# Kernel tuning notes

Hardware: AMD Instinct MI355X
Metric: run time of the kernel (lower is better)

The kernel has to match this reference:

```python
import jax, jax.numpy as jnp
import numpy as np

G, BATCH, L, S_D, I_D, O_D = 2, 128, 2048, 64, 16, 16
SNR = 10.0


def _stable_F(key):
    # mirror utils.sample_stable_state_matrix: random matrix with spectral radius < 1
    A = jax.random.normal(key, (G, S_D, S_D), jnp.float32)
    sig_max = jnp.linalg.svd(A, compute_uv=False)[..., 0]  # spectral norm >= spectral radius
    return 0.95 * A / sig_max[:, None, None]


def setup_inputs() -> dict:
    key = jax.random.key(0)
    ks = jax.random.split(key, 9)
    return {
        "state": jax.random.normal(ks[0], (G, BATCH, S_D), jnp.float32),
        "inputs": jax.random.normal(ks[1], (G, BATCH, L, I_D), jnp.float32),
        "F": _stable_F(ks[2]),
        "B_mat": jax.random.normal(ks[3], (G, S_D, I_D), jnp.float32),
        "H": jax.random.normal(ks[4], (G, O_D, S_D), jnp.float32),
        "sqrt_S_W": jax.random.normal(ks[5], (G, S_D, S_D), jnp.float32) / SNR,
        "sqrt_S_V": jax.random.normal(ks[6], (G, O_D, O_D), jnp.float32) / SNR,
        "w_noise": jax.random.normal(ks[7], (L, G, BATCH, S_D), jnp.float32),
        "v_noise": jax.random.normal(ks[8], (L, G, BATCH, O_D), jnp.float32),
    }


def reference(state, inputs, F, B_mat, H, sqrt_S_W, sqrt_S_V, w_noise, v_noise):
    # Color the noise: randn @ sqrt_S.mT, as in the torch forward
    W = jnp.einsum('lgbs,gts->lgbt', w_noise, sqrt_S_W)   # [L,G,B,S_D]
    V = jnp.einsum('lgbo,gpo->lgbp', v_noise, sqrt_S_V)   # [L,G,B,O_D]
    # Precompute input drive for every step: inputs_ @ B.mT
    Bu = jnp.einsum('gbli,gsi->lgbs', inputs, B_mat)      # [L,G,B,S_D]

    def step(s, xs):
        Bu_t, W_t, V_t = xs
        s = jnp.einsum('gbs,gts->gbt', s, F) + Bu_t + W_t  # state @ F.mT + u @ B.mT + W
        o = jnp.einsum('gbs,gos->gbo', s, H) + V_t         # state @ H.mT + V
        return s, (s, o)

    _, (states, observations) = jax.lax.scan(step, state, (Bu, W, V))
    # [L,G,B,D] -> [G,B,L,D] to match torch.stack(..., dim=-2)
    states = jnp.moveaxis(states, 0, -2)
    observations = jnp.moveaxis(observations, 0, -2)
    return states, observations
```

## Files before the change

### kernel.cpp

```cpp
#include <hip/hip_runtime.h>

#define G_ 2
#define B_ 128
#define L_ 2048
#define SD 64
#define ID 16
#define OD 16
#define NC4 512
#define OBS_BASE ((size_t)(G_) * B_ * L_ * SD)

typedef float v2 __attribute__((ext_vector_type(2)));

static __device__ __forceinline__ size_t slotof(int g, int b, int l) {
  return (((size_t)g * B_ + b) * L_ + l) * (size_t)SD;
}
static __device__ __forceinline__ size_t oslot(int g, int b, int c4) {
  return OBS_BASE + (((size_t)g * B_ + b) * L_ + (size_t)c4 * 4) * OD;
}
static __device__ __forceinline__ float rl(float v, int lane) {
  return __builtin_bit_cast(float, __builtin_amdgcn_readlane(__builtin_bit_cast(int, v), lane));
}
static __device__ __forceinline__ void lds_barrier() {
  asm volatile("s_waitcnt lgkmcnt(0)\n\ts_barrier" ::: "memory");
}

static __device__ void lds_sq(const float* A, float* C, int tid) {
  const int r = tid & 63, q = tid >> 6;
  const float4* Ar = (const float4*)(A + r * SD);
  float acc[16];
#pragma unroll
  for (int c = 0; c < 16; ++c) acc[c] = 0.f;
#pragma unroll 1
  for (int k4 = 0; k4 < 16; ++k4) {
    float4 af = Ar[k4];
    const float* Bb = A + k4 * 4 * SD + q * 16;
#pragma unroll
    for (int kk = 0; kk < 4; ++kk) {
      float a = (kk == 0) ? af.x : (kk == 1) ? af.y : (kk == 2) ? af.z : af.w;
      const float4* Bk = (const float4*)(Bb + kk * SD);
#pragma unroll
      for (int c = 0; c < 4; ++c) {
        float4 bv = Bk[c];
        acc[4 * c + 0] = fmaf(a, bv.x, acc[4 * c + 0]);
        acc[4 * c + 1] = fmaf(a, bv.y, acc[4 * c + 1]);
        acc[4 * c + 2] = fmaf(a, bv.z, acc[4 * c + 2]);
        acc[4 * c + 3] = fmaf(a, bv.w, acc[4 * c + 3]);
      }
    }
  }
  float4* Cr = (float4*)(C + r * SD + q * 16);
#pragma unroll
  for (int c = 0; c < 4; ++c)
    Cr[c] = make_float4(acc[4 * c], acc[4 * c + 1], acc[4 * c + 2], acc[4 * c + 3]);
}

__global__ __launch_bounds__(256) void kPre(
    const float* __restrict__ wn, const float* __restrict__ inp,
    const float* __restrict__ SW, const float* __restrict__ Bm,
    float* __restrict__ out) {
  __shared__ __align__(16) float Mt[80 * 64];
  __shared__ __align__(16) float Nt[80 * 64];
  const int tid = threadIdx.x;
  const int bid = (int)blockIdx.x;
  const int g = bid >> 12;
  const int rem = bid & 4095;
  const int l = rem >> 1;
  const int b0 = (rem & 1) * 64;
  {
    const int row = tid >> 2;
    const int k0 = (tid & 3) * 16;
    const float4* sp = (const float4*)(SW + (g * SD + row) * SD + k0);
#pragma unroll
    for (int q = 0; q < 4; ++q) {
      float4 v = sp[q];
      Mt[(k0 + 4 * q + 0) * 64 + row] = v.x;
      Mt[(k0 + 4 * q + 1) * 64 + row] = v.y;
      Mt[(k0 + 4 * q + 2) * 64 + row] = v.z;
      Mt[(k0 + 4 * q + 3) * 64 + row] = v.w;
    }
    const int k2 = (tid & 3) * 4;
    float4 bv = *(const float4*)(Bm + (g * SD + row) * ID + k2);
    Mt[(64 + k2 + 0) * 64 + row] = bv.x;
    Mt[(64 + k2 + 1) * 64 + row] = bv.y;
    Mt[(64 + k2 + 2) * 64 + row] = bv.z;
    Mt[(64 + k2 + 3) * 64 + row] = bv.w;
  }
  {
    const int item = tid & 63;
    const int kq = tid >> 6;
    const float4* wp =
        (const float4*)(wn + (((size_t)l * G_ + g) * B_ + b0 + item) * SD + kq * 16);
#pragma unroll
    for (int q = 0; q < 4; ++q) {
      float4 v = wp[q];
      const int k = kq * 16 + 4 * q;
      Nt[(k + 0) * 64 + item] = v.x;
      Nt[(k + 1) * 64 + item] = v.y;
      Nt[(k + 2) * 64 + item] = v.z;
      Nt[(k + 3) * 64 + item] = v.w;
    }
    const int item2 = tid >> 2;
    const int k2 = (tid & 3) * 4;
    float4 uv = *(const float4*)(inp + (((size_t)g * B_ + b0 + item2) * L_ + l) * ID + k2);
    Nt[(64 + k2 + 0) * 64 + item2] = uv.x;
    Nt[(64 + k2 + 1) * 64 + item2] = uv.y;
    Nt[(64 + k2 + 2) * 64 + item2] = uv.z;
    Nt[(64 + k2 + 3) * 64 + item2] = uv.w;
  }
  __syncthreads();
  const int i0 = (tid & 15) * 4;
  const int r0 = (tid >> 4) * 4;
  float acc[4][4];
#pragma unroll
  for (int r = 0; r < 4; ++r)
#pragma unroll
    for (int i = 0; i < 4; ++i) acc[r][i] = 0.f;
#pragma unroll 4
  for (int k = 0; k < 80; ++k) {
    float4 a = *(const float4*)(Mt + k * 64 + r0);
    float4 w = *(const float4*)(Nt + k * 64 + i0);
    float ar[4] = {a.x, a.y, a.z, a.w};
    float wi[4] = {w.x, w.y, w.z, w.w};
#pragma unroll
    for (int r = 0; r < 4; ++r)
#pragma unroll
      for (int i = 0; i < 4; ++i) acc[r][i] = fmaf(ar[r], wi[i], acc[r][i]);
  }
#pragma unroll
  for (int i = 0; i < 4; ++i) {
    float4 v = make_float4(acc[0][i], acc[1][i], acc[2][i], acc[3][i]);
    *(float4*)(out + slotof(g, b0 + i0 + i, l) + r0) = v;
  }
}

__global__ __launch_bounds__(256, 2) void kA(const float* __restrict__ Fm,
                                             float* __restrict__ out) {
  __shared__ __align__(16) float zb[SD * 64];
  const int tid = threadIdx.x;
  const int bid = (int)blockIdx.x;
  const int c4 = bid & (NC4 - 1);
  const int half = (bid >> 9) & 1;
  const int g = bid >> 10;
  const int l0 = c4 * 4;
  const int lane = tid & 63;
  const int ww = __builtin_amdgcn_readfirstlane(tid >> 6);
  const int b = half * 64 + lane;
  const int row0 = ww * 16;
  const float* __restrict__ Fg = Fm + g * SD * SD;

  v2 z2[32];
  {
    const float4* ip = (const float4*)(out + slotof(g, b, l0));
#pragma unroll
    for (int q = 0; q < 16; ++q) {
      float4 f = ip[q];
      z2[2 * q] = (v2){f.x, f.y};
      z2[2 * q + 1] = (v2){f.z, f.w};
    }
  }
  float4 d4[4];
  {
    const float4* dp = (const float4*)(out + slotof(g, b, l0 + 1) + row0);
#pragma unroll
    for (int q = 0; q < 4; ++q) d4[q] = dp[q];
  }

#pragma unroll 1
  for (int j = 1; j < 4; ++j) {
    if (j != 1) lds_barrier();
#pragma unroll
    for (int c = 0; c < 16; ++c) {
      const int row = row0 + c;
      const float4* fr = (const float4*)(Fg + row * SD);
      v2 a0 = {0.f, 0.f}, a1 = {0.f, 0.f}, a2 = {0.f, 0.f}, a3 = {0.f, 0.f};
#pragma unroll
      for (int q = 0; q < 16; ++q) {
        float4 f = fr[q];
        if (q & 1) {
          a2 += (v2){f.x, f.y} * z2[2 * q];
          a3 += (v2){f.z, f.w} * z2[2 * q + 1];
        } else {
          a0 += (v2){f.x, f.y} * z2[2 * q];
          a1 += (v2){f.z, f.w} * z2[2 * q + 1];
        }
      }
      v2 aa = (a0 + a1) + (a2 + a3);
      float dv = ((c & 3) == 0) ? d4[c >> 2].x
               : ((c & 3) == 1) ? d4[c >> 2].y
               : ((c & 3) == 2) ? d4[c >> 2].z : d4[c >> 2].w;
      zb[row * 64 + lane] = aa.x + aa.y + dv;
    }
    float4 d4n[4];
    if (j != 3) {
      const float4* dp = (const float4*)(out + slotof(g, b, l0 + j + 1) + row0);
#pragma unroll
      for (int q = 0; q < 4; ++q) d4n[q] = dp[q];
    }
    lds_barrier();
    if (j != 3) {
#pragma unroll
      for (int k = 0; k < 32; ++k)
        z2[k] = (v2){zb[(2 * k) * 64 + lane], zb[(2 * k + 1) * 64 + lane]};
#pragma unroll
      for (int q = 0; q < 4; ++q) d4[q] = d4n[q];
    }
  }
  {
    const int item = tid & 63;
    const int kg = tid >> 6;
    float* dst = out + oslot(g, half * 64 + item, c4);
#pragma unroll
    for (int r = 0; r < 4; ++r) {
      float4 v;
      v.x = zb[(kg * 16 + 4 * r + 0) * 64 + item];
      v.y = zb[(kg * 16 + 4 * r + 1) * 64 + item];
      v.z = zb[(kg * 16 + 4 * r + 2) * 64 + item];
      v.w = zb[(kg * 16 + 4 * r + 3) * 64 + item];
      ((float4*)dst)[kg * 4 + r] = v;
    }
  }
}

__global__ __launch_bounds__(256) void kBscan(const float* __restrict__ Fm,
                                              const float* __restrict__ s0,
                                              float* __restrict__ out) {
  __shared__ __align__(16) float bufA[SD * SD];
  __shared__ __align__(16) float bufB[SD * SD];
  const int tid = threadIdx.x;
  const int gb = (int)blockIdx.x * 4 + (tid >> 6);
  const int g = gb >> 7, b = gb & 127;
  const int lane = tid & 63;
  {
    const int gg = ((int)blockIdx.x * 4) >> 7;
    const float4* Fg = (const float4*)(Fm + gg * SD * SD);
    float4* A4 = (float4*)bufA;
    for (int i = tid; i < SD * SD / 4; i += 256) A4[i] = Fg[i];
  }
  __syncthreads();
  lds_sq(bufA, bufB, tid);  __syncthreads();
  lds_sq(bufB, bufA, tid);  __syncthreads();

  float frow[SD];
  const float4* Fr = (const float4*)(bufA + lane * SD);
#pragma unroll
  for (int i = 0; i < 16; ++i) {
    float4 f = Fr[i];
    frow[4 * i] = f.x; frow[4 * i + 1] = f.y; frow[4 * i + 2] = f.z; frow[4 * i + 3] = f.w;
  }
  float* base = out + oslot(g, b, 0);
  float s = s0[(g * B_ + b) * SD + lane];
  float zcur = base[0 * 64 + lane];
  float znext = base[1 * 64 + lane];
#pragma unroll 1
  for (int c4 = 0; c4 < NC4; ++c4) {
    asm volatile("s_waitcnt vmcnt(0)" ::: "memory");
    base[(size_t)c4 * 64 + lane] = s;
    const int cn = (c4 + 2 < NC4) ? c4 + 2 : NC4 - 1;
    float zpf = base[(size_t)cn * 64 + lane];
    float a0 = zcur, a1 = 0.f, a2 = 0.f, a3 = 0.f;
#pragma unroll
    for (int k = 0; k < SD; k += 4) {
      a0 = fmaf(frow[k + 0], rl(s, k + 0), a0);
      a1 = fmaf(frow[k + 1], rl(s, k + 1), a1);
      a2 = fmaf(frow[k + 2], rl(s, k + 2), a2);
      a3 = fmaf(frow[k + 3], rl(s, k + 3), a3);
    }
    s = (a0 + a1) + (a2 + a3);
    zcur = znext;
    znext = zpf;
  }
}

__global__ __launch_bounds__(256, 2) void kC(
    const float* __restrict__ vn, const float* __restrict__ Fm,
    const float* __restrict__ Hm, const float* __restrict__ SV,
    float* __restrict__ out) {
  __shared__ __align__(16) float zb[SD * 64];
  __shared__ __align__(16) float ob[OD * 64];
  const int tid = threadIdx.x;
  const int bid = (int)blockIdx.x;
  const int c4 = bid & (NC4 - 1);
  const int half = (bid >> 9) & 1;
  const int g = bid >> 10;
  const int l0 = c4 * 4;
  const int lane = tid & 63;
  const int ww = __builtin_amdgcn_readfirstlane(tid >> 6);
  const int b = half * 64 + lane;
  const int row0 = ww * 16;
  const int item = tid & 63;
  const int kg = tid >> 6;
  const float* __restrict__ Fg = Fm + g * SD * SD;
  const float* __restrict__ Hg = Hm + g * OD * SD;
  const float* __restrict__ Vg = SV + g * OD * OD;

  v2 z2[32];
  {
    const float4* ip = (const float4*)(out + oslot(g, b, c4));
#pragma unroll
    for (int q = 0; q < 16; ++q) {
      float4 f = ip[q];
      z2[2 * q] = (v2){f.x, f.y};
      z2[2 * q + 1] = (v2){f.z, f.w};
    }
  }
  float4 d4[4];
  v2 vv2[8];
  {
    const float4* dp = (const float4*)(out + slotof(g, b, l0) + row0);
#pragma unroll
    for (int q = 0; q < 4; ++q) d4[q] = dp[q];
    const v2* vp = (const v2*)(vn + (((size_t)l0 * G_ + g) * B_ + b) * OD);
#pragma unroll
    for (int q = 0; q < 8; ++q) vv2[q] = vp[q];
  }

#pragma unroll 1
  for (int j = 0; j < 4; ++j) {
    const int l = l0 + j;
#pragma unroll
    for (int c = 0; c < 16; ++c) {
      const int row = row0 + c;
      const float4* fr = (const float4*)(Fg + row * SD);
      v2 a0 = {0.f, 0.f}, a1 = {0.f, 0.f}, a2 = {0.f, 0.f}, a3 = {0.f, 0.f};
#pragma unroll
      for (int q = 0; q < 16; ++q) {
        float4 f = fr[q];
        if (q & 1) {
          a2 += (v2){f.x, f.y} * z2[2 * q];
          a3 += (v2){f.z, f.w} * z2[2 * q + 1];
        } else {
          a0 += (v2){f.x, f.y} * z2[2 * q];
          a1 += (v2){f.z, f.w} * z2[2 * q + 1];
        }
      }
      v2 aa = (a0 + a1) + (a2 + a3);
      float dv = ((c & 3) == 0) ? d4[c >> 2].x
               : ((c & 3) == 1) ? d4[c >> 2].y
               : ((c & 3) == 2) ? d4[c >> 2].z : d4[c >> 2].w;
      zb[row * 64 + lane] = aa.x + aa.y + dv;
    }
    float4 d4n[4];
    v2 vvn[8];
    if (j != 3) {
      const float4* dp = (const float4*)(out + slotof(g, b, l + 1) + row0);
#pragma unroll
      for (int q = 0; q < 4; ++q) d4n[q] = dp[q];
      const v2* vp = (const v2*)(vn + (((size_t)(l + 1) * G_ + g) * B_ + b) * OD);
#pragma unroll
      for (int q = 0; q < 8; ++q) vvn[q] = vp[q];
    }
    lds_barrier();
    {
      float* dst = out + slotof(g, half * 64 + item, l);
#pragma unroll
      for (int r = 0; r < 4; ++r) {
        float4 v;
        v.x = zb[(kg * 16 + 4 * r + 0) * 64 + item];
        v.y = zb[(kg * 16 + 4 * r + 1) * 64 + item];
        v.z = zb[(kg * 16 + 4 * r + 2) * 64 + item];
        v.w = zb[(kg * 16 + 4 * r + 3) * 64 + item];
        ((float4*)dst)[kg * 4 + r] = v;
      }
    }
#pragma unroll
    for (int k = 0; k < 32; ++k)
      z2[k] = (v2){zb[(2 * k) * 64 + lane], zb[(2 * k + 1) * 64 + lane]};
#pragma unroll
    for (int oc = 0; oc < 4; ++oc) {
      const int orow = ww * 4 + oc;
      const float4* hr = (const float4*)(Hg + orow * SD);
      const float4* vr = (const float4*)(Vg + orow * OD);
      v2 a0 = {0.f, 0.f}, a1 = {0.f, 0.f};
#pragma unroll
      for (int q = 0; q < 16; ++q) {
        float4 h = hr[q];
        a0 += (v2){h.x, h.y} * z2[2 * q];
        a1 += (v2){h.z, h.w} * z2[2 * q + 1];
      }
#pragma unroll
      for (int q = 0; q < 4; ++q) {
        float4 sv = vr[q];
        a0 += (v2){sv.x, sv.y} * vv2[2 * q];
        a1 += (v2){sv.z, sv.w} * vv2[2 * q + 1];
      }
      v2 aa = a0 + a1;
      ob[orow * 64 + lane] = aa.x + aa.y;
    }
    lds_barrier();
    {
      float4 v;
      v.x = ob[(4 * kg + 0) * 64 + item];
      v.y = ob[(4 * kg + 1) * 64 + item];
      v.z = ob[(4 * kg + 2) * 64 + item];
      v.w = ob[(4 * kg + 3) * 64 + item];
      float* od = out + OBS_BASE +
                  (((size_t)g * B_ + (half * 64 + item)) * L_ + l) * OD;
      ((float4*)od)[kg] = v;
    }
    if (j != 3) {
#pragma unroll
      for (int q = 0; q < 4; ++q) d4[q] = d4n[q];
#pragma unroll
      for (int q = 0; q < 8; ++q) vv2[q] = vvn[q];
    }
  }
}

extern "C" void kernel_launch(void* const* d_in, const int* in_sizes, int n_in,
                              void* d_out, int out_size, void* d_ws, size_t ws_size,
                              hipStream_t stream) {
  (void)in_sizes; (void)n_in; (void)out_size; (void)d_ws; (void)ws_size;
  const float* state0 = (const float*)d_in[0];
  const float* inputs = (const float*)d_in[1];
  const float* Fm     = (const float*)d_in[2];
  const float* Bm     = (const float*)d_in[3];
  const float* Hm     = (const float*)d_in[4];
  const float* SW     = (const float*)d_in[5];
  const float* SV     = (const float*)d_in[6];
  const float* wn     = (const float*)d_in[7];
  const float* vn     = (const float*)d_in[8];
  float* out = (float*)d_out;

  kPre<<<8192, 256, 0, stream>>>(wn, inputs, SW, Bm, out);
  kA<<<2048, 256, 0, stream>>>(Fm, out);
  kBscan<<<64, 256, 0, stream>>>(Fm, state0, out);
  kC<<<2048, 256, 0, stream>>>(vn, Fm, Hm, SV, out);
}
```

Before: 766.5 us.

## Split sequential block scan into parallel chunked scan with carry propagation

Replaces the per-(g,b) single-wave sequential scan over 512 blocked steps with a three-phase chunked scan. Sixteen waves each scan 32 steps from zero, one wave propagates carries using F^(4*32) computed by repeated LDS squaring, then all waves rescan with the correct starting state. It also switches the inner matvec to packed FMA with SGPR operands and pads LDS rows to avoid bank conflicts. This aims to cut the long serial dependency chain and raise occupancy, at the cost of doubling the scan arithmetic and adding several extra matrix squarings.

```diff
diff --git a/kernel.cpp b/kernel.cpp
--- a/kernel.cpp
+++ b/kernel.cpp
@@ -7,6 +7,7 @@
 #define ID 16
 #define OD 16
 #define NC4 512
+#define ROWP 68
 #define OBS_BASE ((size_t)(G_) * B_ * L_ * SD)
 
 typedef float v2 __attribute__((ext_vector_type(2)));
@@ -20,24 +21,42 @@
 static __device__ __forceinline__ float rl(float v, int lane) {
   return __builtin_bit_cast(float, __builtin_amdgcn_readlane(__builtin_bit_cast(int, v), lane));
 }
+static __device__ __forceinline__ void pkfma_s(v2& acc, v2 m, v2 z) {
+  asm("v_pk_fma_f32 %0, %1, %2, %0" : "+v"(acc) : "s"(m), "v"(z));
+}
 static __device__ __forceinline__ void lds_barrier() {
   asm volatile("s_waitcnt lgkmcnt(0)\n\ts_barrier" ::: "memory");
 }
 
-static __device__ void lds_sq(const float* A, float* C, int tid) {
+static __device__ __forceinline__ float a_step(const v2 (&fr2)[32], float s, float add) {
+  v2 a0 = {add, 0.f}, a1 = {0.f, 0.f}, a2 = {0.f, 0.f}, a3 = {0.f, 0.f};
+#pragma unroll
+  for (int k2 = 0; k2 < 32; ++k2) {
+    v2 m;
+    m.x = rl(s, 2 * k2);
+    m.y = rl(s, 2 * k2 + 1);
+    if ((k2 & 3) == 0)      pkfma_s(a0, m, fr2[k2]);
+    else if ((k2 & 3) == 1) pkfma_s(a1, m, fr2[k2]);
+    else if ((k2 & 3) == 2) pkfma_s(a2, m, fr2[k2]);
+    else                    pkfma_s(a3, m, fr2[k2]);
+  }
+  v2 aa = (a0 + a1) + (a2 + a3);
+  return aa.x + aa.y;
+}
+
+static __device__ void lds_sq_p(const float* A, float* C, int tid) {
   const int r = tid & 63, q = tid >> 6;
-  const float4* Ar = (const float4*)(A + r * SD);
+  const float4* Ar = (const float4*)(A + r * ROWP);
   float acc[16];
 #pragma unroll
   for (int c = 0; c < 16; ++c) acc[c] = 0.f;
 #pragma unroll 1
   for (int k4 = 0; k4 < 16; ++k4) {
     float4 af = Ar[k4];
-    const float* Bb = A + k4 * 4 * SD + q * 16;
 #pragma unroll
     for (int kk = 0; kk < 4; ++kk) {
       float a = (kk == 0) ? af.x : (kk == 1) ? af.y : (kk == 2) ? af.z : af.w;
-      const float4* Bk = (const float4*)(Bb + kk * SD);
+      const float4* Bk = (const float4*)(A + (k4 * 4 + kk) * ROWP + q * 16);
 #pragma unroll
       for (int c = 0; c < 4; ++c) {
         float4 bv = Bk[c];
@@ -48,7 +67,7 @@
       }
     }
   }
-  float4* Cr = (float4*)(C + r * SD + q * 16);
+  float4* Cr = (float4*)(C + r * ROWP + q * 16);
 #pragma unroll
   for (int c = 0; c < 4; ++c)
     Cr[c] = make_float4(acc[4 * c], acc[4 * c + 1], acc[4 * c + 2], acc[4 * c + 3]);
@@ -221,53 +240,104 @@
   }
 }
 
-__global__ __launch_bounds__(256) void kBscan(const float* __restrict__ Fm,
-                                              const float* __restrict__ s0,
-                                              float* __restrict__ out) {
-  __shared__ __align__(16) float bufA[SD * SD];
-  __shared__ __align__(16) float bufB[SD * SD];
+__global__ __launch_bounds__(1024, 4) void kBscan2(const float* __restrict__ Fm,
+                                                   const float* __restrict__ s0,
+                                                   float* __restrict__ out) {
+  __shared__ __align__(16) float bufA[SD * ROWP];
+  __shared__ __align__(16) float bufB[SD * ROWP];
+  __shared__ float carr[16][64];
+  __shared__ float gbuf[16][64];
   const int tid = threadIdx.x;
-  const int gb = (int)blockIdx.x * 4 + (tid >> 6);
-  const int g = gb >> 7, b = gb & 127;
+  const int bid = (int)blockIdx.x;
+  const int g = bid >> 7;
+  const int b = bid & 127;
   const int lane = tid & 63;
-  {
-    const int gg = ((int)blockIdx.x * 4) >> 7;
-    const float4* Fg = (const float4*)(Fm + gg * SD * SD);
-    float4* A4 = (float4*)bufA;
-    for (int i = tid; i < SD * SD / 4; i += 256) A4[i] = Fg[i];
-  }
-  __syncthreads();
-  lds_sq(bufA, bufB, tid);  __syncthreads();
-  lds_sq(bufB, bufA, tid);  __syncthreads();
-
-  float frow[SD];
-  const float4* Fr = (const float4*)(bufA + lane * SD);
-#pragma unroll
-  for (int i = 0; i < 16; ++i) {
-    float4 f = Fr[i];
-    frow[4 * i] = f.x; frow[4 * i + 1] = f.y; frow[4 * i + 2] = f.z; frow[4 * i + 3] = f.w;
-  }
+  const int w = __builtin_amdgcn_readfirstlane(tid >> 6);
+
+  {
+    const float* Fg = Fm + g * SD * SD;
+    for (int i = tid; i < SD * SD; i += 1024)
+      bufA[(i >> 6) * ROWP + (i & 63)] = Fg[i];
+  }
+  __syncthreads();
+  if (tid < 256) lds_sq_p(bufA, bufB, tid);
+  __syncthreads();
+  if (tid < 256) lds_sq_p(bufB, bufA, tid);
+  __syncthreads();
+  v2 fr2[32];
+  {
+    const v2* rp = (const v2*)(bufA + lane * ROWP);
+#pragma unroll
+    for (int k = 0; k < 32; ++k) fr2[k] = rp[k];
+  }
+  __syncthreads();
+  if (tid < 256) lds_sq_p(bufA, bufB, tid);
+  __syncthreads();
+  if (tid < 256) lds_sq_p(bufB, bufA, tid);
+  __syncthreads();
+  if (tid < 256) lds_sq_p(bufA, bufB, tid);
+  __syncthreads();
+  if (tid < 256) lds_sq_p(bufB, bufA, tid);
+  __syncthreads();
+  if (tid < 256) lds_sq_p(bufA, bufB, tid);
+  __syncthreads();
+
   float* base = out + oslot(g, b, 0);
-  float s = s0[(g * B_ + b) * SD + lane];
-  float zcur = base[0 * 64 + lane];
-  float znext = base[1 * 64 + lane];
-#pragma unroll 1
-  for (int c4 = 0; c4 < NC4; ++c4) {
-    asm volatile("s_waitcnt vmcnt(0)" ::: "memory");
-    base[(size_t)c4 * 64 + lane] = s;
-    const int cn = (c4 + 2 < NC4) ? c4 + 2 : NC4 - 1;
-    float zpf = base[(size_t)cn * 64 + lane];
-    float a0 = zcur, a1 = 0.f, a2 = 0.f, a3 = 0.f;
-#pragma unroll
-    for (int k = 0; k < SD; k += 4) {
-      a0 = fmaf(frow[k + 0], rl(s, k + 0), a0);
-      a1 = fmaf(frow[k + 1], rl(s, k + 1), a1);
-      a2 = fmaf(frow[k + 2], rl(s, k + 2), a2);
-      a3 = fmaf(frow[k + 3], rl(s, k + 3), a3);
-    }
-    s = (a0 + a1) + (a2 + a3);
-    zcur = znext;
-    znext = zpf;
+  const int c0 = w * 32;
+
+  {
+    float s = 0.f;
+    float z0 = base[(size_t)c0 * 64 + lane];
+    float z1 = base[(size_t)(c0 + 1) * 64 + lane];
+#pragma unroll 1
+    for (int i = 0; i < 32; ++i) {
+      const int cn = (i + 2 < 32) ? c0 + i + 2 : c0 + 31;
+      float zpf = base[(size_t)cn * 64 + lane];
+      s = a_step(fr2, s, z0);
+      z0 = z1;
+      z1 = zpf;
+    }
+    carr[w][lane] = s;
+  }
+  __syncthreads();
+  if (w == 0) {
+    const float* arow = bufB + lane * ROWP;
+    float G = s0[(g * B_ + b) * SD + lane];
+#pragma unroll 1
+    for (int m = 0; m < 16; ++m) {
+      gbuf[m][lane] = G;
+      v2 a0 = {carr[m][lane], 0.f}, a1 = {0.f, 0.f}, a2 = {0.f, 0.f}, a3 = {0.f, 0.f};
+#pragma unroll
+      for (int k2 = 0; k2 < 32; ++k2) {
+        v2 mr = ((const v2*)arow)[k2];
+        v2 mm;
+        mm.x = rl(G, 2 * k2);
+        mm.y = rl(G, 2 * k2 + 1);
+        if ((k2 & 3) == 0)      pkfma_s(a0, mm, mr);
+        else if ((k2 & 3) == 1) pkfma_s(a1, mm, mr);
+        else if ((k2 & 3) == 2) pkfma_s(a2, mm, mr);
+        else                    pkfma_s(a3, mm, mr);
+      }
+      v2 aa = (a0 + a1) + (a2 + a3);
+      G = aa.x + aa.y;
+    }
+  }
+  __syncthreads();
+  {
+    float s = gbuf[w][lane];
+    float zcur = base[(size_t)c0 * 64 + lane];
+    float znext = base[(size_t)(c0 + 1) * 64 + lane];
+#pragma unroll 1
+    for (int i = 0; i < 32; ++i) {
+      const int c = c0 + i;
+      asm volatile("s_waitcnt vmcnt(0)" ::: "memory");
+      base[(size_t)c * 64 + lane] = s;
+      const int cn = (i + 2 < 32) ? c + 2 : c0 + 31;
+      float zpf = base[(size_t)cn * 64 + lane];
+      s = a_step(fr2, s, zcur);
+      zcur = znext;
+      znext = zpf;
+    }
   }
 }
 
@@ -423,6 +493,6 @@
 
   kPre<<<8192, 256, 0, stream>>>(wn, inputs, SW, Bm, out);
   kA<<<2048, 256, 0, stream>>>(Fm, out);
-  kBscan<<<64, 256, 0, stream>>>(Fm, state0, out);
+  kBscan2<<<256, 1024, 0, stream>>>(Fm, state0, out);
   kC<<<2048, 256, 0, stream>>>(vn, Fm, Hm, SV, out);
 }
```

After: 657.4 us. 1.17x faster.
